# Kernel tuning notes

Hardware: AMD Instinct MI355X
Metric: run time of the kernel (lower is better)

## Reference

```python
import jax, jax.numpy as jnp
import numpy as np

B = 8192
LOD = 60      # latent_obs_dim
LSD = 2 * LOD # latent state dim
AD = 10       # act_dim
NB = 15       # num_basis
BW = 3        # bandwidth
H = 60        # control-net hidden units


def elup1(x):
    # exp(x) if x < 0 else x + 1 (positive covariance activation)
    return jnp.where(x < 0.0, jnp.exp(x), x + 1.0)


def setup_inputs() -> dict:
    key = jax.random.key(0)
    ks = jax.random.split(key, 16)
    inp = {
        "post_mean": jax.random.normal(ks[0], (B, LSD), jnp.float32),
        "cu": jax.random.uniform(ks[1], (B, LOD), jnp.float32) + 0.1,
        "cl": jax.random.uniform(ks[2], (B, LOD), jnp.float32) + 0.1,
        "cs": 0.01 * jax.random.normal(ks[3], (B, LOD), jnp.float32),
        "action": jax.random.normal(ks[4], (B, AD), jnp.float32),
        # transition basis matrices (params); original init is zeros/+-0.2*I,
        # use small random values for a non-degenerate numerical test
        "tm11": 0.05 * jax.random.normal(ks[5], (NB, LOD, LOD), jnp.float32),
        "tm12": 0.2 * jnp.eye(LOD)[None] + 0.02 * jax.random.normal(ks[6], (NB, LOD, LOD), jnp.float32),
        "tm21": -0.2 * jnp.eye(LOD)[None] + 0.02 * jax.random.normal(ks[7], (NB, LOD, LOD), jnp.float32),
        "tm22": 0.05 * jax.random.normal(ks[8], (NB, LOD, LOD), jnp.float32),
        # log transition noise, init elup1_inv(1.0) = 0.0 -> perturb slightly
        "log_noise": 0.1 * jax.random.normal(ks[9], (1, LSD), jnp.float32),
        # coefficient net: Linear(LSD -> NB) + Softmax (no hidden layers)
        "w_coef": jax.random.normal(ks[10], (NB, LSD), jnp.float32) / np.sqrt(LSD),
        "b_coef": jnp.zeros((NB,), jnp.float32),
        # control net: Linear(AD -> H) + ReLU + Linear(H -> LSD)
        "w_c1": jax.random.normal(ks[11], (H, AD), jnp.float32) / np.sqrt(AD),
        "b_c1": jnp.zeros((H,), jnp.float32),
        "w_c2": jax.random.normal(ks[12], (LSD, H), jnp.float32) / np.sqrt(H),
        "b_c2": jnp.zeros((LSD,), jnp.float32),
    }
    return inp


def _band_mask():
    idx = jnp.arange(LOD)
    return (jnp.abs(idx[:, None] - idx[None, :]) <= BW).astype(jnp.float32)


def reference(post_mean, cu, cl, cs, action,
              tm11, tm12, tm21, tm22, log_noise,
              w_coef, b_coef, w_c1, b_c1, w_c2, b_c2):
    mask = _band_mask()            # [LOD, LOD]
    eye = jnp.eye(LOD, dtype=post_mean.dtype)

    # coefficient net + softmax -> basis-weighted transition matrices
    coef = jax.nn.softmax(post_mean @ w_coef.T + b_coef, axis=-1)  # [B, NB]

    def mix(tm):  # [B, LOD, LOD], band-masked
        return jnp.einsum('bk,kij->bij', coef, tm) * mask

    t11 = mix(tm11) + eye
    t12 = mix(tm12)
    t21 = mix(tm21)
    t22 = mix(tm22) + eye

    # control net contribution
    control = jax.nn.relu(action @ w_c1.T + b_c1) @ w_c2.T + b_c2  # [B, LSD]

    trans_cov = elup1(log_noise)        # [1, LSD]
    tc_u = trans_cov[..., :LOD]
    tc_l = trans_cov[..., LOD:]

    mu = post_mean[:, :LOD]
    ml = post_mean[:, LOD:]

    bmv = lambda m, v: jnp.einsum('bij,bj->bi', m, v)

    nmu = bmv(t11, mu) + bmv(t12, ml)
    nml = bmv(t21, mu) + bmv(t22, ml)

    # diagonal covariance predict (dadat / dadbt)
    ncu = bmv(t11 ** 2, cu) + 2.0 * bmv(t11 * t12, cs) + bmv(t12 ** 2, cl) + tc_u
    ncl = bmv(t21 ** 2, cu) + 2.0 * bmv(t21 * t22, cs) + bmv(t22 ** 2, cl) + tc_l
    ncs = bmv(t21 * t11, cu) + bmv(t22 * t11, cs) + bmv(t21 * t12, cs) + bmv(t22 * t12, cl)

    next_mean = jnp.concatenate([nmu, nml], axis=-1) + control
    return (next_mean, ncu, ncl, ncs)
```

## Files before the change

kernel.cpp:

```cpp
#include <hip/hip_runtime.h>
#include <math.h>

#define BATCH 8192
#define LOD 60
#define LSD 120
#define AD 10
#define NB 15
#define BW 3
#define H 60

#define NM_SZ (BATCH * LSD)
#define NC_SZ (BATCH * LOD)

#define TMBG_STRIDE 448
#define TMBG_ROW 420
#define TMBG_FLOATS (LOD * TMBG_STRIDE)

#define RGS 8
#define RG_ROWS 8
#define NJJ 16
#define VSJ 65
#define VSV (NJJ * VSJ)
#define VS_FLOATS (5 * VSV)
#define COEF_OFF VS_FLOATS
#define HID_OFF (VS_FLOATS + NB * 64)
#define OST_OFF VS_FLOATS
#define OST_PLANE (RG_ROWS * 65)
#define OVL_FLOATS (VS_FLOATS + 4860)

typedef float v2f __attribute__((ext_vector_type(2)));
#define FMA2(a, b, c) __builtin_elementwise_fma((a), (b), (c))

__device__ __forceinline__ float elup1f(float x) {
    return x < 0.0f ? __expf(x) : x + 1.0f;
}

__global__ __launch_bounds__(256) void k_pack(
    const float* __restrict__ tm11, const float* __restrict__ tm12,
    const float* __restrict__ tm21, const float* __restrict__ tm22,
    float* __restrict__ tmbg)
{
    int idx = blockIdx.x * 256 + threadIdx.x;
    if (idx >= TMBG_FLOATS) return;
    int i = idx / TMBG_STRIDE;
    int r = idx - i * TMBG_STRIDE;
    float val = 0.0f;
    if (r < TMBG_ROW) {
        int k  = r / 28;
        int z  = r - k * 28;
        int jo = z >> 2;
        int m  = z & 3;
        int j  = i - BW + jo;
        const float* tmm = (m == 0) ? tm11 : (m == 1) ? tm12 : (m == 2) ? tm21 : tm22;
        if (j >= 0 && j < LOD) val = tmm[k * (LOD * LOD) + i * LOD + j];
    }
    tmbg[idx] = val;
}

__global__ __launch_bounds__(256, 4) void k_fused(
    const float* __restrict__ pm, const float* __restrict__ cu,
    const float* __restrict__ cl, const float* __restrict__ cs,
    const float* __restrict__ action,
    const float* __restrict__ log_noise,
    const float* __restrict__ w_coef, const float* __restrict__ b_coef,
    const float* __restrict__ w_c1, const float* __restrict__ b_c1,
    const float* __restrict__ w_c2, const float* __restrict__ b_c2,
    const float* __restrict__ tmbg,
    float* __restrict__ out)
{
    __shared__ __align__(16) float ovl[OVL_FLOATS];

    const int tid  = threadIdx.x;
    const int lane = tid & 63;
    const int wv   = __builtin_amdgcn_readfirstlane(tid >> 6);

    const int bid  = blockIdx.x;
    const int xcd  = bid & 7;
    const int slot = bid >> 3;
    const int bg   = xcd * 16 + (slot >> 3);
    const int rg   = slot & 7;
    const int b0   = bg * 64;
    const int i0   = rg * RG_ROWS;

    float* vsb   = ovl;
    float* coefL = ovl + COEF_OFF;
    float* hid_s = ovl + HID_OFF;

    float vr[20];
    {
        const int jj  = tid & 15;
        const int j   = i0 - BW + jj;
        const bool jok = (j >= 0) && (j < LOD);
        #pragma unroll
        for (int z = 0; z < 20; ++z) {
            const int idx = z * 256 + tid;
            const int blc = (idx >> 4) & 63;
            const int bb  = b0 + blc;
            float val = 0.0f;
            if (jok) {
                const int v = z >> 2;
                if (v == 0)      val = pm[bb * LSD + j];
                else if (v == 1) val = pm[bb * LSD + LOD + j];
                else if (v == 2) val = cu[bb * LOD + j];
                else if (v == 3) val = cl[bb * LOD + j];
                else             val = cs[bb * LOD + j];
            }
            vr[z] = val;
        }
    }

    {
        const int k0 = wv, k1 = wv + 4, k2 = wv + 8;
        const int k3 = (wv < 3) ? wv + 12 : 14;
        const float4* pmv = (const float4*)(pm + (size_t)(b0 + lane) * LSD);
        const float4* w0 = (const float4*)(w_coef + k0 * LSD);
        const float4* w1 = (const float4*)(w_coef + k1 * LSD);
        const float4* w2 = (const float4*)(w_coef + k2 * LSD);
        const float4* w3 = (const float4*)(w_coef + k3 * LSD);
        v2f a0 = {0.f, 0.f}, a1 = {0.f, 0.f}, a2 = {0.f, 0.f}, a3 = {0.f, 0.f};
        #pragma unroll 6
        for (int d = 0; d < LSD / 4; ++d) {
            float4 p = pmv[d];
            v2f plo = {p.x, p.y}, phi = {p.z, p.w};
            float4 u0 = w0[d], u1 = w1[d], u2 = w2[d], u3 = w3[d];
            a0 = FMA2(plo, ((v2f){u0.x, u0.y}), a0);
            a0 = FMA2(phi, ((v2f){u0.z, u0.w}), a0);
            a1 = FMA2(plo, ((v2f){u1.x, u1.y}), a1);
            a1 = FMA2(phi, ((v2f){u1.z, u1.w}), a1);
            a2 = FMA2(plo, ((v2f){u2.x, u2.y}), a2);
            a2 = FMA2(phi, ((v2f){u2.z, u2.w}), a2);
            a3 = FMA2(plo, ((v2f){u3.x, u3.y}), a3);
            a3 = FMA2(phi, ((v2f){u3.z, u3.w}), a3);
        }
        coefL[k0 * 64 + lane] = a0.x + a0.y + b_coef[k0];
        coefL[k1 * 64 + lane] = a1.x + a1.y + b_coef[k1];
        coefL[k2 * 64 + lane] = a2.x + a2.y + b_coef[k2];
        if (wv < 3) coefL[k3 * 64 + lane] = a3.x + a3.y + b_coef[k3];
    }
    {
        v2f av2[5];
        const float2* a2p = (const float2*)(action + (size_t)(b0 + lane) * AD);
        #pragma unroll
        for (int z = 0; z < 5; ++z) { float2 t2 = a2p[z]; av2[z] = (v2f){t2.x, t2.y}; }
        #pragma unroll
        for (int q = 0; q < 15; ++q) {
            int h = wv * 15 + q;
            v2f acc2 = {0.f, 0.f};
            #pragma unroll
            for (int z = 0; z < 5; ++z)
                acc2 = FMA2(av2[z], *(const v2f*)(w_c1 + h * AD + 2 * z), acc2);
            float acc = acc2.x + acc2.y + b_c1[h];
            hid_s[h * 65 + lane] = fmaxf(acc, 0.0f);
        }
    }
    __syncthreads();

    float cf[NB];
    {
        float mx = -1e30f;
        #pragma unroll
        for (int k = 0; k < NB; ++k) { cf[k] = coefL[k * 64 + lane]; mx = fmaxf(mx, cf[k]); }
        float sm = 0.0f;
        #pragma unroll
        for (int k = 0; k < NB; ++k) { cf[k] = __expf(cf[k] - mx); sm += cf[k]; }
        float inv = 1.0f / sm;
        #pragma unroll
        for (int k = 0; k < NB; ++k) cf[k] *= inv;
    }
    const int r0g = i0 + 2 * wv;
    const int c0  = (r0g < LOD) ? r0g : LOD - 1;
    const int c1  = (r0g + 1 < LOD) ? r0g + 1 : LOD - 1;
    float ctl0 = b_c2[c0], ctl1 = b_c2[c1];
    float ctl2 = b_c2[LOD + c0], ctl3 = b_c2[LOD + c1];
    #pragma unroll 4
    for (int h = 0; h < H; ++h) {
        float hv = hid_s[h * 65 + lane];
        ctl0 = fmaf(hv, w_c2[c0 * H + h], ctl0);
        ctl1 = fmaf(hv, w_c2[c1 * H + h], ctl1);
        ctl2 = fmaf(hv, w_c2[(LOD + c0) * H + h], ctl2);
        ctl3 = fmaf(hv, w_c2[(LOD + c1) * H + h], ctl3);
    }

    {
        const int jj = tid & 15;
        #pragma unroll
        for (int z = 0; z < 20; ++z) {
            const int idx = z * 256 + tid;
            const int blc = (idx >> 4) & 63;
            vsb[(z >> 2) * VSV + jj * VSJ + blc] = vr[z];
        }
    }
    __syncthreads();

    float onm[2], onl[2], ouv[2], olv[2], osv[2];
    #pragma unroll
    for (int rr = 0; rr < 2; ++rr) {
        const int riu = 2 * wv + rr;
        const int iu  = i0 + riu;
        const int iuc = (iu < LOD) ? iu : LOD - 1;

        const float* tpg = tmbg + (size_t)iuc * TMBG_STRIDE;
        v2f t2[14];
        #pragma unroll
        for (int z = 0; z < 14; ++z) t2[z] = (v2f){0.f, 0.f};
        #pragma unroll
        for (int k = 0; k < NB; ++k) {
            v2f c2 = {cf[k], cf[k]};
            #pragma unroll
            for (int jo = 0; jo < 7; ++jo) {
                v2f w01 = *(const v2f*)(tpg + k * 28 + jo * 4);
                v2f w23 = *(const v2f*)(tpg + k * 28 + jo * 4 + 2);
                t2[2 * jo]     = FMA2(c2, w01, t2[2 * jo]);
                t2[2 * jo + 1] = FMA2(c2, w23, t2[2 * jo + 1]);
            }
        }
        t2[6].x += 1.0f;
        t2[7].y += 1.0f;

        float nmu = 0.f, nml = 0.f, ncuv = 0.f, nclv = 0.f, ncsv = 0.f;
        #pragma unroll
        for (int jo = 0; jo < 7; ++jo) {
            const int jj = riu + jo;
            float m_ = vsb[0 * VSV + jj * VSJ + lane];
            float n_ = vsb[1 * VSV + jj * VSJ + lane];
            float u_ = vsb[2 * VSV + jj * VSJ + lane];
            float l_ = vsb[3 * VSV + jj * VSJ + lane];
            float s_ = vsb[4 * VSV + jj * VSJ + lane];
            float A  = t2[2 * jo].x,     Bv = t2[2 * jo].y;
            float C  = t2[2 * jo + 1].x, D  = t2[2 * jo + 1].y;
            nmu = fmaf(A, m_, nmu);  nmu = fmaf(Bv, n_, nmu);
            nml = fmaf(C, m_, nml);  nml = fmaf(D, n_, nml);
            float e1 = fmaf(Bv, s_, A * u_);
            float e2 = fmaf(Bv, l_, A * s_);
            float f1 = fmaf(D, s_, C * u_);
            float f2 = fmaf(D, l_, C * s_);
            ncuv = fmaf(A, e1, ncuv);  ncuv = fmaf(Bv, e2, ncuv);
            nclv = fmaf(C, f1, nclv);  nclv = fmaf(D, f2, nclv);
            ncsv = fmaf(C, e1, ncsv);  ncsv = fmaf(D, e2, ncsv);
        }
        ncuv += elup1f(log_noise[iuc]);
        nclv += elup1f(log_noise[LOD + iuc]);
        nmu  += (rr == 0) ? ctl0 : ctl1;
        nml  += (rr == 0) ? ctl2 : ctl3;
        onm[rr] = nmu; onl[rr] = nml; ouv[rr] = ncuv; olv[rr] = nclv; osv[rr] = ncsv;
    }

    float* ost = ovl + OST_OFF;
    #pragma unroll
    for (int rr = 0; rr < 2; ++rr) {
        const int ri = 2 * wv + rr;
        ost[0 * OST_PLANE + ri * 65 + lane] = onm[rr];
        ost[1 * OST_PLANE + ri * 65 + lane] = onl[rr];
        ost[2 * OST_PLANE + ri * 65 + lane] = ouv[rr];
        ost[3 * OST_PLANE + ri * 65 + lane] = olv[rr];
        ost[4 * OST_PLANE + ri * 65 + lane] = osv[rr];
    }
    __syncthreads();

    for (int idx = tid; idx < 5 * 64 * 2; idx += 256) {
        int q   = idx & 1;
        int blc = (idx >> 1) & 63;
        int t5  = idx >> 7;
        if (i0 + q * 4 + 3 >= LOD) continue;
        int bb = b0 + blc;
        int ro = q * 4;
        float4 v;
        v.x = ost[t5 * OST_PLANE + (ro + 0) * 65 + blc];
        v.y = ost[t5 * OST_PLANE + (ro + 1) * 65 + blc];
        v.z = ost[t5 * OST_PLANE + (ro + 2) * 65 + blc];
        v.w = ost[t5 * OST_PLANE + (ro + 3) * 65 + blc];
        float* bp;
        if (t5 == 0)      bp = out + bb * LSD + i0;
        else if (t5 == 1) bp = out + bb * LSD + LOD + i0;
        else if (t5 == 2) bp = out + NM_SZ + bb * LOD + i0;
        else if (t5 == 3) bp = out + NM_SZ + NC_SZ + bb * LOD + i0;
        else              bp = out + NM_SZ + 2 * NC_SZ + bb * LOD + i0;
        *(float4*)(bp + ro) = v;
    }
}

extern "C" void kernel_launch(void* const* d_in, const int* in_sizes, int n_in,
                              void* d_out, int out_size, void* d_ws, size_t ws_size,
                              hipStream_t stream) {
    (void)in_sizes; (void)n_in; (void)out_size; (void)ws_size;
    const float* pm        = (const float*)d_in[0];
    const float* cu        = (const float*)d_in[1];
    const float* cl        = (const float*)d_in[2];
    const float* cs        = (const float*)d_in[3];
    const float* action    = (const float*)d_in[4];
    const float* tm11      = (const float*)d_in[5];
    const float* tm12      = (const float*)d_in[6];
    const float* tm21      = (const float*)d_in[7];
    const float* tm22      = (const float*)d_in[8];
    const float* log_noise = (const float*)d_in[9];
    const float* w_coef    = (const float*)d_in[10];
    const float* b_coef    = (const float*)d_in[11];
    const float* w_c1      = (const float*)d_in[12];
    const float* b_c1      = (const float*)d_in[13];
    const float* w_c2      = (const float*)d_in[14];
    const float* b_c2      = (const float*)d_in[15];

    float* tmbg = (float*)d_ws;

    hipLaunchKernelGGL(k_pack, dim3((TMBG_FLOATS + 255) / 256), dim3(256), 0, stream,
                       tm11, tm12, tm21, tm22, tmbg);

    hipLaunchKernelGGL(k_fused, dim3(1024), dim3(256), 0, stream,
                       pm, cu, cl, cs, action, log_noise,
                       w_coef, b_coef, w_c1, b_c1, w_c2, b_c2, tmbg,
                       (float*)d_out);
}
```

Baseline: 116.6 us.

## Hoist softmax coefficients and control net into a separate prep kernel

Moves the coefficient-net softmax and the control MLP out of the fused kernel into a prep kernel that runs once per batch tile. The prep kernel also packs the transition bases and writes the results to workspace. The main kernel then loads the per-batch coefficients and control values instead of recomputing them in each of the 8 row-group blocks. This removes redundant matvec work and shrinks the main kernel's shared-memory use, at the cost of extra global memory traffic through the workspace.

```diff
diff --git a/kernel.cpp b/kernel.cpp
--- a/kernel.cpp
+++ b/kernel.cpp
@@ -15,6 +15,8 @@
 #define TMBG_STRIDE 448
 #define TMBG_ROW 420
 #define TMBG_FLOATS (LOD * TMBG_STRIDE)
+#define WS_COEF TMBG_FLOATS
+#define WS_CTRL (WS_COEF + NB * BATCH)
 
 #define RGS 8
 #define RG_ROWS 8
@@ -22,11 +24,7 @@
 #define VSJ 65
 #define VSV (NJJ * VSJ)
 #define VS_FLOATS (5 * VSV)
-#define COEF_OFF VS_FLOATS
-#define HID_OFF (VS_FLOATS + NB * 64)
-#define OST_OFF VS_FLOATS
 #define OST_PLANE (RG_ROWS * 65)
-#define OVL_FLOATS (VS_FLOATS + 4860)
 
 typedef float v2f __attribute__((ext_vector_type(2)));
 #define FMA2(a, b, c) __builtin_elementwise_fma((a), (b), (c))
@@ -35,79 +33,45 @@
     return x < 0.0f ? __expf(x) : x + 1.0f;
 }
 
-__global__ __launch_bounds__(256) void k_pack(
+__global__ __launch_bounds__(256) void k_prep(
+    const float* __restrict__ pm, const float* __restrict__ action,
     const float* __restrict__ tm11, const float* __restrict__ tm12,
     const float* __restrict__ tm21, const float* __restrict__ tm22,
-    float* __restrict__ tmbg)
-{
-    int idx = blockIdx.x * 256 + threadIdx.x;
-    if (idx >= TMBG_FLOATS) return;
-    int i = idx / TMBG_STRIDE;
-    int r = idx - i * TMBG_STRIDE;
-    float val = 0.0f;
-    if (r < TMBG_ROW) {
-        int k  = r / 28;
-        int z  = r - k * 28;
-        int jo = z >> 2;
-        int m  = z & 3;
-        int j  = i - BW + jo;
-        const float* tmm = (m == 0) ? tm11 : (m == 1) ? tm12 : (m == 2) ? tm21 : tm22;
-        if (j >= 0 && j < LOD) val = tmm[k * (LOD * LOD) + i * LOD + j];
-    }
-    tmbg[idx] = val;
-}
-
-__global__ __launch_bounds__(256, 4) void k_fused(
-    const float* __restrict__ pm, const float* __restrict__ cu,
-    const float* __restrict__ cl, const float* __restrict__ cs,
-    const float* __restrict__ action,
-    const float* __restrict__ log_noise,
     const float* __restrict__ w_coef, const float* __restrict__ b_coef,
     const float* __restrict__ w_c1, const float* __restrict__ b_c1,
     const float* __restrict__ w_c2, const float* __restrict__ b_c2,
-    const float* __restrict__ tmbg,
-    float* __restrict__ out)
+    float* __restrict__ ws)
 {
-    __shared__ __align__(16) float ovl[OVL_FLOATS];
-
-    const int tid  = threadIdx.x;
+    const int tid = threadIdx.x;
+    const int bid = blockIdx.x;
+
+    if (bid >= 128) {
+        int idx = (bid - 128) * 256 + tid;
+        if (idx < TMBG_FLOATS) {
+            int i = idx / TMBG_STRIDE;
+            int r = idx - i * TMBG_STRIDE;
+            float val = 0.0f;
+            if (r < TMBG_ROW) {
+                int k  = r / 28;
+                int z  = r - k * 28;
+                int jo = z >> 2;
+                int m  = z & 3;
+                int j  = i - BW + jo;
+                const float* tmm = (m == 0) ? tm11 : (m == 1) ? tm12
+                                 : (m == 2) ? tm21 : tm22;
+                if (j >= 0 && j < LOD) val = tmm[k * (LOD * LOD) + i * LOD + j];
+            }
+            ws[idx] = val;
+        }
+        return;
+    }
+
+    __shared__ float lg_s[NB * 64];
+    __shared__ float hid_s[H * 65];
+
     const int lane = tid & 63;
     const int wv   = __builtin_amdgcn_readfirstlane(tid >> 6);
-
-    const int bid  = blockIdx.x;
-    const int xcd  = bid & 7;
-    const int slot = bid >> 3;
-    const int bg   = xcd * 16 + (slot >> 3);
-    const int rg   = slot & 7;
-    const int b0   = bg * 64;
-    const int i0   = rg * RG_ROWS;
-
-    float* vsb   = ovl;
-    float* coefL = ovl + COEF_OFF;
-    float* hid_s = ovl + HID_OFF;
-
-    float vr[20];
-    {
-        const int jj  = tid & 15;
-        const int j   = i0 - BW + jj;
-        const bool jok = (j >= 0) && (j < LOD);
-        #pragma unroll
-        for (int z = 0; z < 20; ++z) {
-            const int idx = z * 256 + tid;
-            const int blc = (idx >> 4) & 63;
-            const int bb  = b0 + blc;
-            float val = 0.0f;
-            if (jok) {
-                const int v = z >> 2;
-                if (v == 0)      val = pm[bb * LSD + j];
-                else if (v == 1) val = pm[bb * LSD + LOD + j];
-                else if (v == 2) val = cu[bb * LOD + j];
-                else if (v == 3) val = cl[bb * LOD + j];
-                else             val = cs[bb * LOD + j];
-            }
-            vr[z] = val;
-        }
-    }
+    const int b0   = bid * 64;
 
     {
         const int k0 = wv, k1 = wv + 4, k2 = wv + 8;
@@ -132,10 +96,10 @@
             a3 = FMA2(plo, ((v2f){u3.x, u3.y}), a3);
             a3 = FMA2(phi, ((v2f){u3.z, u3.w}), a3);
         }
-        coefL[k0 * 64 + lane] = a0.x + a0.y + b_coef[k0];
-        coefL[k1 * 64 + lane] = a1.x + a1.y + b_coef[k1];
-        coefL[k2 * 64 + lane] = a2.x + a2.y + b_coef[k2];
-        if (wv < 3) coefL[k3 * 64 + lane] = a3.x + a3.y + b_coef[k3];
+        lg_s[k0 * 64 + lane] = a0.x + a0.y + b_coef[k0];
+        lg_s[k1 * 64 + lane] = a1.x + a1.y + b_coef[k1];
+        lg_s[k2 * 64 + lane] = a2.x + a2.y + b_coef[k2];
+        if (wv < 3) lg_s[k3 * 64 + lane] = a3.x + a3.y + b_coef[k3];
     }
     {
         v2f av2[5];
@@ -155,30 +119,93 @@
     }
     __syncthreads();
 
+    if (tid < 64) {
+        float v[NB];
+        float mx = -1e30f;
+        #pragma unroll
+        for (int k = 0; k < NB; ++k) { v[k] = lg_s[k * 64 + tid]; mx = fmaxf(mx, v[k]); }
+        float sm = 0.0f;
+        #pragma unroll
+        for (int k = 0; k < NB; ++k) { v[k] = __expf(v[k] - mx); sm += v[k]; }
+        float inv = 1.0f / sm;
+        #pragma unroll
+        for (int k = 0; k < NB; ++k) ws[WS_COEF + k * BATCH + b0 + tid] = v[k] * inv;
+    }
+
+    {
+        float acc[30];
+        #pragma unroll
+        for (int q = 0; q < 30; ++q) acc[q] = b_c2[wv * 30 + q];
+        for (int h = 0; h < H; ++h) {
+            float hv = hid_s[h * 65 + lane];
+            #pragma unroll
+            for (int q = 0; q < 30; ++q)
+                acc[q] = fmaf(hv, w_c2[(wv * 30 + q) * H + h], acc[q]);
+        }
+        #pragma unroll
+        for (int q = 0; q < 30; ++q)
+            ws[WS_CTRL + (wv * 30 + q) * BATCH + b0 + lane] = acc[q];
+    }
+}
+
+__global__ __launch_bounds__(256, 4) void k_main(
+    const float* __restrict__ pm, const float* __restrict__ cu,
+    const float* __restrict__ cl, const float* __restrict__ cs,
+    const float* __restrict__ log_noise,
+    const float* __restrict__ ws,
+    float* __restrict__ out)
+{
+    __shared__ __align__(16) float vsb[VS_FLOATS];
+
+    const int tid  = threadIdx.x;
+    const int lane = tid & 63;
+    const int wv   = __builtin_amdgcn_readfirstlane(tid >> 6);
+
+    const int bid  = blockIdx.x;
+    const int xcd  = bid & 7;
+    const int slot = bid >> 3;
+    const int bg   = xcd * 16 + (slot >> 3);
+    const int rg   = slot & 7;
+    const int b0   = bg * 64;
+    const int i0   = rg * RG_ROWS;
+    const int b    = b0 + lane;
+
+    const float* coef_t = ws + WS_COEF;
+    const float* ctrl_t = ws + WS_CTRL;
+
     float cf[NB];
-    {
-        float mx = -1e30f;
-        #pragma unroll
-        for (int k = 0; k < NB; ++k) { cf[k] = coefL[k * 64 + lane]; mx = fmaxf(mx, cf[k]); }
-        float sm = 0.0f;
-        #pragma unroll
-        for (int k = 0; k < NB; ++k) { cf[k] = __expf(cf[k] - mx); sm += cf[k]; }
-        float inv = 1.0f / sm;
-        #pragma unroll
-        for (int k = 0; k < NB; ++k) cf[k] *= inv;
-    }
+    #pragma unroll
+    for (int k = 0; k < NB; ++k) cf[k] = coef_t[k * BATCH + b];
+
     const int r0g = i0 + 2 * wv;
     const int c0  = (r0g < LOD) ? r0g : LOD - 1;
     const int c1  = (r0g + 1 < LOD) ? r0g + 1 : LOD - 1;
-    float ctl0 = b_c2[c0], ctl1 = b_c2[c1];
-    float ctl2 = b_c2[LOD + c0], ctl3 = b_c2[LOD + c1];
-    #pragma unroll 4
-    for (int h = 0; h < H; ++h) {
-        float hv = hid_s[h * 65 + lane];
-        ctl0 = fmaf(hv, w_c2[c0 * H + h], ctl0);
-        ctl1 = fmaf(hv, w_c2[c1 * H + h], ctl1);
-        ctl2 = fmaf(hv, w_c2[(LOD + c0) * H + h], ctl2);
-        ctl3 = fmaf(hv, w_c2[(LOD + c1) * H + h], ctl3);
+    float ctl0 = ctrl_t[c0 * BATCH + b];
+    float ctl1 = ctrl_t[c1 * BATCH + b];
+    float ctl2 = ctrl_t[(LOD + c0) * BATCH + b];
+    float ctl3 = ctrl_t[(LOD + c1) * BATCH + b];
+
+    float vr[20];
+    {
+        const int jj  = tid & 15;
+        const int j   = i0 - BW + jj;
+        const bool jok = (j >= 0) && (j < LOD);
+        #pragma unroll
+        for (int z = 0; z < 20; ++z) {
+            const int idx = z * 256 + tid;
+            const int blc = (idx >> 4) & 63;
+            const int bb  = b0 + blc;
+            float val = 0.0f;
+            if (jok) {
+                const int v = z >> 2;
+                if (v == 0)      val = pm[bb * LSD + j];
+                else if (v == 1) val = pm[bb * LSD + LOD + j];
+                else if (v == 2) val = cu[bb * LOD + j];
+                else if (v == 3) val = cl[bb * LOD + j];
+                else             val = cs[bb * LOD + j];
+            }
+            vr[z] = val;
+        }
     }
 
     {
@@ -199,7 +226,7 @@
         const int iu  = i0 + riu;
         const int iuc = (iu < LOD) ? iu : LOD - 1;
 
-        const float* tpg = tmbg + (size_t)iuc * TMBG_STRIDE;
+        const float* tpg = ws + (size_t)iuc * TMBG_STRIDE;
         v2f t2[14];
         #pragma unroll
         for (int z = 0; z < 14; ++z) t2[z] = (v2f){0.f, 0.f};
@@ -244,8 +271,9 @@
         nml  += (rr == 0) ? ctl2 : ctl3;
         onm[rr] = nmu; onl[rr] = nml; ouv[rr] = ncuv; olv[rr] = nclv; osv[rr] = ncsv;
     }
-
-    float* ost = ovl + OST_OFF;
+    __syncthreads();
+
+    float* ost = vsb;
     #pragma unroll
     for (int rr = 0; rr < 2; ++rr) {
         const int ri = 2 * wv + rr;
@@ -300,13 +328,12 @@
     const float* w_c2      = (const float*)d_in[14];
     const float* b_c2      = (const float*)d_in[15];
 
-    float* tmbg = (float*)d_ws;
-
-    hipLaunchKernelGGL(k_pack, dim3((TMBG_FLOATS + 255) / 256), dim3(256), 0, stream,
-                       tm11, tm12, tm21, tm22, tmbg);
-
-    hipLaunchKernelGGL(k_fused, dim3(1024), dim3(256), 0, stream,
-                       pm, cu, cl, cs, action, log_noise,
-                       w_coef, b_coef, w_c1, b_c1, w_c2, b_c2, tmbg,
-                       (float*)d_out);
+    float* ws = (float*)d_ws;
+
+    hipLaunchKernelGGL(k_prep, dim3(128 + TMBG_FLOATS / 256), dim3(256), 0, stream,
+                       pm, action, tm11, tm12, tm21, tm22,
+                       w_coef, b_coef, w_c1, b_c1, w_c2, b_c2, ws);
+
+    hipLaunchKernelGGL(k_main, dim3(1024), dim3(256), 0, stream,
+                       pm, cu, cl, cs, log_noise, ws, (float*)d_out);
 }
```

Result: slower. 153.2 us (+31.4%).
